# Performance work log

Measured on AMD Instinct MI355X. Metric: run time of the kernel, lower is better.

Reference implementation:

```python
import jax, jax.numpy as jnp
import numpy as np
from jax import lax

CONF_THRES = 0.25
IOU_THRES = 0.45
MAX_DET = 300      # detections kept after NMS
TOPK = 1024        # candidates entering NMS (sorted by score)
MAX_WH = 7680.0    # class offset for class-aware NMS
NC = 80            # classes
NM = 32            # mask prototypes
IMG = 640          # network input size
PROTO_HW = 160     # proto map resolution (IMG/4)
EPS = 1e-7


def xywh2xyxy(x):
    cx, cy, w, h = x[:, 0], x[:, 1], x[:, 2], x[:, 3]
    return jnp.stack([cx - w / 2, cy - h / 2, cx + w / 2, cy + h / 2], axis=1)


def box_iou(box1, box2):
    # box1: [K,4], box2: [M,4] in xyxy -> [K,M]
    a1, a2 = box1[:, None, :2], box1[:, None, 2:]
    b1, b2 = box2[None, :, :2], box2[None, :, 2:]
    inter = jnp.clip(jnp.minimum(a2, b2) - jnp.maximum(a1, b1), 0).prod(-1)
    area1 = (a2 - a1).prod(-1)
    area2 = (b2 - b1).prod(-1)
    return inter / (area1 + area2 - inter + EPS)


def greedy_nms_keep(boxes, valid, iou_thres):
    # boxes already sorted by descending score; returns bool keep mask [K]
    K = boxes.shape[0]
    sup = box_iou(boxes, boxes) > iou_thres  # [K,K]
    lower = jnp.arange(K)

    def body(i, keep):
        suppressed = jnp.any(keep & sup[:, i] & (lower < i))
        return keep.at[i].set(valid[i] & ~suppressed)

    return lax.fori_loop(0, K, body, jnp.zeros((K,), dtype=bool))


def setup_inputs() -> dict:
    key = jax.random.key(0)
    k1, k2, k3, k4, k5, k6 = jax.random.split(key, 6)
    N = 25200
    cxcy = jax.random.uniform(k1, (1, N, 2), jnp.float32, 0.0, float(IMG))
    wh = jax.random.uniform(k2, (1, N, 2), jnp.float32, 5.0, 120.0)
    obj = jax.random.uniform(k3, (1, N, 1), jnp.float32)
    cls = jax.random.uniform(k4, (1, N, NC), jnp.float32)
    coef = jax.random.normal(k5, (1, N, NM), jnp.float32) * 0.5
    prediction = jnp.concatenate([cxcy, wh, obj, cls, coef], axis=2)  # [1,N,117]
    protos = jax.random.normal(k6, (NM, PROTO_HW, PROTO_HW), jnp.float32)
    return {"prediction": prediction, "protos": protos}


def reference(prediction, protos):
    x = prediction[0]                       # [N, 5+NC+NM]
    obj = x[:, 4]
    cls_conf = x[:, 5:5 + NC] * obj[:, None]  # x[:,5:] *= x[:,4:5]
    conf = cls_conf.max(axis=1)
    j = jnp.argmax(cls_conf, axis=1)
    valid_all = (obj > CONF_THRES) & (conf > CONF_THRES)

    boxes_all = xywh2xyxy(x[:, :4])
    scores_masked = jnp.where(valid_all, conf, -1.0)
    top_scores, idx = lax.top_k(scores_masked, TOPK)  # sorted descending

    b = boxes_all[idx]              # [TOPK,4], no class offset
    cls_id = j[idx]                 # [TOPK]
    coef = x[idx, 5 + NC:]          # [TOPK,NM]
    valid = top_scores > CONF_THRES

    nms_boxes = b + (cls_id.astype(b.dtype) * MAX_WH)[:, None]  # class-aware
    keep = greedy_nms_keep(nms_boxes, valid, IOU_THRES)

    keep_scores = jnp.where(keep, top_scores, -1.0)
    fs, i2 = lax.top_k(keep_scores, MAX_DET)
    fvalid = fs > CONF_THRES
    fb = b[i2] * fvalid[:, None].astype(b.dtype)
    fcls = jnp.where(fvalid, cls_id[i2], -1)
    fcoef = coef[i2] * fvalid[:, None].astype(coef.dtype)
    fs = jnp.where(fvalid, fs, 0.0)

    # process_mask_native
    m = jax.nn.sigmoid(fcoef @ protos.reshape(NM, -1))          # [MAX_DET, HW*HW]
    m = m.reshape(MAX_DET, PROTO_HW, PROTO_HW)
    m = jax.image.resize(m, (MAX_DET, IMG, IMG), method='bilinear')
    x1, y1, x2, y2 = fb[:, 0], fb[:, 1], fb[:, 2], fb[:, 3]
    r = jnp.arange(IMG, dtype=fb.dtype)[None, None, :]  # along width vs x
    c = jnp.arange(IMG, dtype=fb.dtype)[None, :, None]  # along height vs y
    crop = ((r >= x1[:, None, None]) & (r < x2[:, None, None]) &
            (c >= y1[:, None, None]) & (c < y2[:, None, None]))
    masks_f = m * crop.astype(m.dtype) * fvalid[:, None, None].astype(m.dtype)
    masks_bool = masks_f > 0.5
    return masks_f, masks_bool, fb, fs, fcls
```

## Files before the change

kernel.cpp:

```cpp
#include <hip/hip_runtime.h>

constexpr int   kNA     = 25200;
constexpr int   kStride = 117;
constexpr int   kNC     = 80;
constexpr int   kNM     = 32;
constexpr int   kTopK   = 1024;
constexpr int   kMaxDet = 300;
constexpr int   kImg    = 640;
constexpr int   kPHW    = 160;
constexpr float kConfT  = 0.25f;
constexpr float kIouT   = 0.45f;
constexpr float kMaxWH  = 7680.0f;

constexpr unsigned long long kMaskElems = 300ull * 640ull * 640ull;

typedef float v4f __attribute__((ext_vector_type(4)));

constexpr size_t kN4     = (2ull * kMaskElems) >> 2;
constexpr size_t kZA_end = 27648000;
constexpr size_t kZB_end = 33792000;

constexpr int kZTopk = 512;
constexpr int kZSup  = 256;
constexpr int kZNms  = 1024;

constexpr size_t O_SCORES = 0;
constexpr size_t O_BOXES  = 100864;
constexpr size_t O_CLS    = 504064;
constexpr size_t O_TKIDX  = 604864;
constexpr size_t O_TKSC   = 608960;
constexpr size_t O_TKBOX  = 613056;
constexpr size_t O_TKNBOX = 629440;
constexpr size_t O_TKCLS  = 645824;
constexpr size_t O_SUP    = 649984;
constexpr size_t O_NDET   = 782336;
constexpr size_t O_DBOX   = 782400;
constexpr size_t O_DCOEF  = 787264;

constexpr int kDecRows = 64;
constexpr int kDecThr  = 128;
__global__ __launch_bounds__(kDecThr) void decode_k(const float* __restrict__ pred,
        float* __restrict__ scores, float* __restrict__ boxes, int* __restrict__ cls) {
    __shared__ float rows[kDecRows * kStride];
    int base = blockIdx.x * kDecRows;
    int nrows = min(kDecRows, kNA - base);
    int total = nrows * kStride;
    const float* src = pred + (size_t)base * kStride;
    for (int i = threadIdx.x; i < total; i += kDecThr) rows[i] = src[i];
    __syncthreads();
    int r = threadIdx.x;
    if (r >= nrows) return;
    int a = base + r;
    const float* p = rows + r * kStride;
    float obj = p[4];
    float best = -1.0f; int bj = 0;
    for (int c = 0; c < kNC; ++c) {
        float v = p[5 + c] * obj;
        if (v > best) { best = v; bj = c; }
    }
    bool valid = (obj > kConfT) && (best > kConfT);
    scores[a] = valid ? best : -1.0f;
    float cx = p[0], cy = p[1], w = p[2], h = p[3];
    float hw = w * 0.5f, hh = h * 0.5f;
    boxes[4*a+0] = cx - hw; boxes[4*a+1] = cy - hh;
    boxes[4*a+2] = cx + hw; boxes[4*a+3] = cy + hh;
    cls[a] = bj;
}

__device__ __forceinline__ unsigned f2ord(float f) {
    unsigned b = __float_as_uint(f);
    return (b & 0x80000000u) ? ~b : (b | 0x80000000u);
}
__device__ __forceinline__ float ord2f(unsigned u) {
    unsigned b = (u & 0x80000000u) ? (u ^ 0x80000000u) : ~u;
    return __uint_as_float(b);
}

__global__ __launch_bounds__(1024) void topk_k(const float* __restrict__ scores,
        const float* __restrict__ boxes, const int* __restrict__ cls,
        int* __restrict__ tk_idx, float* __restrict__ tk_sc, float* __restrict__ tk_box,
        float* __restrict__ tk_nbox, int* __restrict__ tk_cls,
        float* __restrict__ outz) {
    if (blockIdx.x != 0) {
        v4f z = 0.f;
        size_t stride = (size_t)(gridDim.x - 1) * 1024;
        for (size_t i = (size_t)(blockIdx.x - 1) * 1024 + threadIdx.x; i < kZA_end; i += stride)
            __builtin_nontemporal_store(z, ((v4f*)outz) + i);
        return;
    }
    __shared__ unsigned long long keys[kTopK];
    __shared__ int wcnt[16];
    __shared__ unsigned sh_cnt;
    int tid = threadIdx.x;
    int lane = tid & 63, wid = tid >> 6;

    unsigned uv[25];
#pragma unroll
    for (int k = 0; k < 25; ++k) {
        int i = tid + k * 1024;
        uv[k] = (i < kNA) ? f2ord(scores[i]) : 0u;
    }

    unsigned lo = 0u, hi = 0xFFFFFFFFu;
    for (int it = 0; it < 34; ++it) {
        unsigned mid;
        if (it == 0)      mid = 0xBE800000u;
        else if (it == 1) mid = 0xBF800001u;
        else {
            mid = (unsigned)(((unsigned long long)lo + (unsigned long long)hi) >> 1);
            if (mid == lo) break;
        }
        if (mid <= lo || mid >= hi) continue;
        int c = 0;
#pragma unroll
        for (int k = 0; k < 25; ++k) c += (uv[k] >= mid);
#pragma unroll
        for (int off = 32; off >= 1; off >>= 1) c += __shfl_down(c, off);
        __syncthreads();
        if (lane == 0) wcnt[wid] = c;
        __syncthreads();
        int tot = 0;
#pragma unroll
        for (int w = 0; w < 16; ++w) tot += wcnt[w];
        if (tot >= kTopK) lo = mid; else hi = mid;
    }
    unsigned uT = lo;

    int nGreater;
    {
        int c = 0;
#pragma unroll
        for (int k = 0; k < 25; ++k) c += (uv[k] >= uT + 1u);
#pragma unroll
        for (int off = 32; off >= 1; off >>= 1) c += __shfl_down(c, off);
        __syncthreads();
        if (lane == 0) wcnt[wid] = c;
        __syncthreads();
        int t = 0;
#pragma unroll
        for (int w = 0; w < 16; ++w) t += wcnt[w];
        nGreater = t;
    }
    int krem = kTopK - nGreater;
    if (tid == 0) sh_cnt = 0;
    __syncthreads();

#pragma unroll
    for (int k = 0; k < 25; ++k) {
        int i = tid + k * 1024;
        unsigned u = uv[k];
        if (i < kNA && u > uT) {
            unsigned p = atomicAdd(&sh_cnt, 1u);
            keys[p] = ((unsigned long long)u << 32) | (unsigned)(~i);
        }
    }

    int ilo = 0, ihi = kNA;
    while (ilo < ihi) {
        int mid = (ilo + ihi) >> 1;
        int c = 0;
#pragma unroll
        for (int k = 0; k < 25; ++k) {
            int i = tid + k * 1024;
            c += (i < mid && uv[k] == uT);
        }
#pragma unroll
        for (int off = 32; off >= 1; off >>= 1) c += __shfl_down(c, off);
        __syncthreads();
        if (lane == 0) wcnt[wid] = c;
        __syncthreads();
        int cc = 0;
#pragma unroll
        for (int w = 0; w < 16; ++w) cc += wcnt[w];
        if (cc >= krem) ihi = mid; else ilo = mid + 1;
    }
#pragma unroll
    for (int k = 0; k < 25; ++k) {
        int i = tid + k * 1024;
        if (i < ilo && uv[k] == uT) {
            unsigned p = atomicAdd(&sh_cnt, 1u);
            keys[p] = ((unsigned long long)uT << 32) | (unsigned)(~i);
        }
    }
    __syncthreads();

    for (int k2 = 2; k2 <= kTopK; k2 <<= 1) {
        for (int j = k2 >> 1; j > 0; j >>= 1) {
            int partner = tid ^ j;
            unsigned long long a = keys[tid], b = keys[partner];
            bool iLower = (tid & j) == 0;
            bool descRegion = (tid & k2) == 0;
            unsigned long long mx = (a > b) ? a : b;
            unsigned long long mn = (a > b) ? b : a;
            unsigned long long res = (iLower == descRegion) ? mx : mn;
            __syncthreads();
            keys[tid] = res;
            __syncthreads();
        }
    }

    unsigned long long key = keys[tid];
    unsigned u = (unsigned)(key >> 32);
    int idx = (int)(~((unsigned)key));
    tk_idx[tid] = idx;
    tk_sc[tid]  = ord2f(u);
    float4 bx = ((const float4*)boxes)[idx];
    ((float4*)tk_box)[tid] = bx;
    int cid = cls[idx];
    float off = (float)cid * kMaxWH;
    float4 nb; nb.x = bx.x + off; nb.y = bx.y + off; nb.z = bx.z + off; nb.w = bx.w + off;
    ((float4*)tk_nbox)[tid] = nb;
    tk_cls[tid] = cid;
}

__global__ __launch_bounds__(256) void supmat_k(const float* __restrict__ tk_nbox,
                                                unsigned long long* __restrict__ sup,
                                                float* __restrict__ outz) {
    if (blockIdx.x >= 64) {
        v4f z = 0.f;
        size_t stride = (size_t)(gridDim.x - 64) * 256;
        for (size_t i = kZA_end + (size_t)(blockIdx.x - 64) * 256 + threadIdx.x;
             i < kZB_end; i += stride)
            __builtin_nontemporal_store(z, ((v4f*)outz) + i);
        return;
    }
    __shared__ float4 bxs[kTopK];
    int tid = threadIdx.x;
    for (int k = tid; k < kTopK; k += 256) bxs[k] = ((const float4*)tk_nbox)[k];
    __syncthreads();
    int r = tid >> 4, w = tid & 15;
    int i = blockIdx.x * 16 + r;
    float4 a = bxs[i];
    float areaA = (a.z - a.x) * (a.w - a.y);
    unsigned long long bits = 0;
    for (int l = 0; l < 64; ++l) {
        float4 b = bxs[w * 64 + l];
        float xx1 = fmaxf(a.x, b.x), yy1 = fmaxf(a.y, b.y);
        float xx2 = fminf(a.z, b.z), yy2 = fminf(a.w, b.w);
        float iw = fmaxf(xx2 - xx1, 0.f), ih = fmaxf(yy2 - yy1, 0.f);
        float inter = iw * ih;
        float areaB = (b.z - b.x) * (b.w - b.y);
        float iou = inter / (areaA + areaB - inter + 1e-7f);
        if (iou > kIouT) bits |= 1ull << l;
    }
    sup[(size_t)i * 16 + w] = bits;
}

__global__ __launch_bounds__(256) void nms_k(const float* __restrict__ pred,
        const float* __restrict__ tk_sc, const int* __restrict__ tk_idx,
        const float* __restrict__ tk_box, const int* __restrict__ tk_cls,
        const unsigned long long* __restrict__ sup,
        int* __restrict__ ndet, float* __restrict__ out,
        float* __restrict__ dbox, float* __restrict__ dcoef) {
    if (blockIdx.x != 0) {
        v4f z = 0.f;
        size_t stride = (size_t)(gridDim.x - 1) * 256;
        for (size_t i = kZB_end + (size_t)(blockIdx.x - 1) * 256 + threadIdx.x;
             i < kN4; i += stride)
            __builtin_nontemporal_store(z, ((v4f*)out) + i);
        return;
    }
    __shared__ unsigned long long buf[2][1024];
    __shared__ int dslot_lds[kMaxDet];
    __shared__ int sh_nd;
    int tid = threadIdx.x;
    int lane = tid & 63;

    unsigned long long vW = 0;
    if (tid < 64) {
        for (int b = 0; b < 16; ++b) {
            unsigned long long bw = __ballot(tk_sc[b * 64 + lane] > kConfT);
            if (lane == b) vW = bw;
        }
    }
    for (int i = tid; i < 1024; i += 256) buf[0][i] = sup[i];

    unsigned long long supW = 0;
    unsigned long long kws[16];
    for (int b = 0; b < 16; ++b) {
        __syncthreads();
        if (tid >= 64) {
            if (b + 1 < 16) {
                for (int i = tid - 64; i < 1024; i += 192)
                    buf[(b + 1) & 1][i] = sup[(size_t)(b + 1) * 1024 + i];
            }
        } else {
            const unsigned long long* ch = buf[b & 1];
            unsigned long long s  = __shfl(supW, b);
            unsigned long long vb = __shfl(vW, b);
            unsigned long long kw = 0;
            unsigned long long rbuf[8];
            int w16 = lane & 15;
#pragma unroll
            for (int p = 0; p < 8; ++p) rbuf[p] = ch[p * 16 + w16];
            for (int l = 0; l < 64; ++l) {
                unsigned long long rw = rbuf[l & 7];
                if (l + 8 < 64) rbuf[l & 7] = ch[(l + 8) * 16 + w16];
                unsigned long long rb = __shfl(rw, b);
                bool kp = ((vb >> l) & 1ull) && !((s >> l) & 1ull);
                if (kp) { kw |= 1ull << l; s |= rb; supW |= rw; }
            }
            kws[b] = kw;
        }
    }
    if (tid == 0) {
        int d = 0;
        for (int b = 0; b < 16 && d < kMaxDet; ++b) {
            unsigned long long kw = kws[b];
            for (int l = 0; l < 64 && d < kMaxDet; ++l)
                if ((kw >> l) & 1ull) dslot_lds[d++] = b * 64 + l;
        }
        sh_nd = d;
        *ndet = d;
    }
    __syncthreads();

    int n = sh_nd;
    float* fb   = out + 2 * kMaskElems;
    float* fs   = fb + kMaxDet * 4;
    float* fcls = fs + kMaxDet;
    for (int d = tid; d < kMaxDet; d += 256) {
        if (d < n) {
            int t = dslot_lds[d];
            int a = tk_idx[t];
            float4 bx = ((const float4*)tk_box)[t];
            fb[4*d+0] = bx.x; fb[4*d+1] = bx.y; fb[4*d+2] = bx.z; fb[4*d+3] = bx.w;
            fs[d] = tk_sc[t];
            fcls[d] = (float)tk_cls[t];
            ((float4*)dbox)[d] = bx;
            const float* cp = pred + (size_t)a * kStride + 5 + kNC;
            for (int c = 0; c < kNM; ++c) dcoef[d * kNM + c] = cp[c];
        } else {
            fb[4*d+0] = 0.f; fb[4*d+1] = 0.f; fb[4*d+2] = 0.f; fb[4*d+3] = 0.f;
            fs[d] = 0.f; fcls[d] = -1.0f;
            float4 z; z.x = z.y = z.z = z.w = 0.f;
            ((float4*)dbox)[d] = z;
            for (int c = 0; c < kNM; ++c) dcoef[d * kNM + c] = 0.f;
        }
    }
}

constexpr int kPatch = 34;

__global__ __launch_bounds__(256) void patch_k(const float* __restrict__ protos,
        const float* __restrict__ dbox, const float* __restrict__ dcoef,
        const int* __restrict__ ndet, float* __restrict__ out) {
    int d = blockIdx.x;
    if (d >= *ndet) return;
    float4 bx = ((const float4*)dbox)[d];
    float x1 = bx.x, y1 = bx.y, x2 = bx.z, y2 = bx.w;

    int i_lo = max(0, (int)ceilf(y1));
    int i_hi = min(kImg - 1, (int)ceilf(y2) - 1);
    int j_lo = max(0, (int)ceilf(x1));
    int j_hi = min(kImg - 1, (int)ceilf(x2) - 1);
    if (i_lo > i_hi || j_lo > j_hi) return;

    int py_lo = min(159, max(0, (int)floorf(((float)i_lo + 0.5f) * 0.25f - 0.5f)));
    int py_hi = min(159, max(0, (int)floorf(((float)i_hi + 0.5f) * 0.25f - 0.5f) + 1));
    int px_lo = min(159, max(0, (int)floorf(((float)j_lo + 0.5f) * 0.25f - 0.5f)));
    int px_hi = min(159, max(0, (int)floorf(((float)j_hi + 0.5f) * 0.25f - 0.5f) + 1));
    int ph = py_hi - py_lo + 1, pw = px_hi - px_lo + 1;
    if (ph > kPatch) ph = kPatch;
    if (pw > kPatch) pw = kPatch;

    int tid = threadIdx.x;
    __shared__ float coef[kNM];
    __shared__ float patch[kPatch * kPatch];
    if (tid < kNM) coef[tid] = dcoef[d * kNM + tid];
    __syncthreads();
    int cells = ph * pw;
    for (int c = tid; c < cells; c += 256) {
        int py = py_lo + c / pw, px = px_lo + c % pw;
        const float* pp = protos + (size_t)py * kPHW + px;
        float z = 0.f;
#pragma unroll
        for (int m = 0; m < kNM; ++m) z = fmaf(coef[m], pp[(size_t)m * kPHW * kPHW], z);
        patch[c] = 1.0f / (1.0f + expf(-z));
    }
    __syncthreads();

    float* mf = out + (size_t)d * (kImg * kImg);
    float* mb = out + kMaskElems + (size_t)d * (kImg * kImg);
    int W = j_hi - j_lo + 1;
    int H = i_hi - i_lo + 1;
    int dr = tid >> 7, dc = tid & 127;
    for (int rr = dr; rr < H; rr += 2) {
        int i = i_lo + rr;
        float sy = fminf(fmaxf(((float)i + 0.5f) * 0.25f - 0.5f, 0.f), 159.f);
        int yy0 = (int)sy; float fy = sy - (float)yy0;
        int yy1i = min(yy0 + 1, 159);
        const float* prow0 = &patch[(yy0 - py_lo) * pw - px_lo];
        const float* prow1 = &patch[(yy1i - py_lo) * pw - px_lo];
        for (int cc = dc; cc < W; cc += 128) {
            int j = j_lo + cc;
            float sx = fminf(fmaxf(((float)j + 0.5f) * 0.25f - 0.5f, 0.f), 159.f);
            int xx0 = (int)sx; float fx = sx - (float)xx0;
            int xx1i = min(xx0 + 1, 159);
            float v00 = prow0[xx0], v01 = prow0[xx1i];
            float v10 = prow1[xx0], v11 = prow1[xx1i];
            float top = (1.f - fx) * v00 + fx * v01;
            float bot = (1.f - fx) * v10 + fx * v11;
            float m = (1.f - fy) * top + fy * bot;
            mf[(size_t)i * kImg + j] = m;
            mb[(size_t)i * kImg + j] = (m > 0.5f) ? 1.f : 0.f;
        }
    }
}

extern "C" void kernel_launch(void* const* d_in, const int* in_sizes, int n_in,
                              void* d_out, int out_size, void* d_ws, size_t ws_size,
                              hipStream_t stream) {
    const float* pred   = (const float*)d_in[0];
    const float* protos = (const float*)d_in[1];
    float* out = (float*)d_out;
    char* ws = (char*)d_ws;

    float* s_scores = (float*)(ws + O_SCORES);
    float* s_boxes  = (float*)(ws + O_BOXES);
    int*   s_cls    = (int*)  (ws + O_CLS);
    int*   tk_idx   = (int*)  (ws + O_TKIDX);
    float* tk_sc    = (float*)(ws + O_TKSC);
    float* tk_box   = (float*)(ws + O_TKBOX);
    float* tk_nbox  = (float*)(ws + O_TKNBOX);
    int*   tk_cls   = (int*)  (ws + O_TKCLS);
    unsigned long long* sup = (unsigned long long*)(ws + O_SUP);
    int*   ndet     = (int*)  (ws + O_NDET);
    float* dbox     = (float*)(ws + O_DBOX);
    float* dcoef    = (float*)(ws + O_DCOEF);

    decode_k<<<dim3((kNA + kDecRows - 1) / kDecRows), dim3(kDecThr), 0, stream>>>(pred, s_scores, s_boxes, s_cls);
    topk_k<<<dim3(1 + kZTopk), dim3(1024), 0, stream>>>(s_scores, s_boxes, s_cls,
                                               tk_idx, tk_sc, tk_box, tk_nbox, tk_cls, out);
    supmat_k<<<dim3(64 + kZSup), dim3(256), 0, stream>>>(tk_nbox, sup, out);
    nms_k<<<dim3(1 + kZNms), dim3(256), 0, stream>>>(pred, tk_sc, tk_idx, tk_box, tk_cls, sup,
                                             ndet, out, dbox, dcoef);
    patch_k<<<dim3(kMaxDet), dim3(256), 0, stream>>>(protos, dbox, dcoef, ndet, out);
}
```

Before: 1.113 ms.

## Skip zero-fill of mask rows covered by boxes; write full rows vectorized

Spreads the zero-fill of the mask output across all five kernels, including decode. The last chunk of the fill now runs in the finalize kernel and skips rows that fall inside each detection's box row range, which nms computes. The patch kernel writes whole 640-wide rows, including the zeros outside the box, as vectorized nontemporal float4 stores. The aim is to avoid writing covered rows twice and to overlap more of the fill with the serial stages, at the cost of extra index arithmetic per fill element.

```diff
diff --git a/kernel.cpp b/kernel.cpp
--- a/kernel.cpp
+++ b/kernel.cpp
@@ -16,13 +16,21 @@
 
 typedef float v4f __attribute__((ext_vector_type(4)));
 
-constexpr size_t kN4     = (2ull * kMaskElems) >> 2;
-constexpr size_t kZA_end = 27648000;
-constexpr size_t kZB_end = 33792000;
-
-constexpr int kZTopk = 512;
-constexpr int kZSup  = 256;
-constexpr int kZNms  = 1024;
+constexpr size_t kN4       = 61440000;
+constexpr size_t kQSlices  = 30720000;
+constexpr int    kQPerSlice= 102400;
+constexpr int    kQPerRow  = 160;
+
+constexpr size_t kZDecE  = 6144000;
+constexpr size_t kZTopkE = 15360000;
+constexpr size_t kZSupE  = 18432000;
+constexpr size_t kZNmsE  = 24576000;
+
+constexpr int kZDecB  = 1024;
+constexpr int kZTopkB = 512;
+constexpr int kZSupB  = 256;
+constexpr int kZNmsB  = 512;
+constexpr int kZFinB  = 1280;
 
 constexpr size_t O_SCORES = 0;
 constexpr size_t O_BOXES  = 100864;
@@ -36,11 +44,22 @@
 constexpr size_t O_NDET   = 782336;
 constexpr size_t O_DBOX   = 782400;
 constexpr size_t O_DCOEF  = 787264;
+constexpr size_t O_ROWR   = 825664;
 
 constexpr int kDecRows = 64;
 constexpr int kDecThr  = 128;
+constexpr int kDecBlocks = (kNA + kDecRows - 1) / kDecRows;
 __global__ __launch_bounds__(kDecThr) void decode_k(const float* __restrict__ pred,
-        float* __restrict__ scores, float* __restrict__ boxes, int* __restrict__ cls) {
+        float* __restrict__ scores, float* __restrict__ boxes, int* __restrict__ cls,
+        float* __restrict__ outz) {
+    if (blockIdx.x >= kDecBlocks) {
+        v4f z = 0.f;
+        size_t stride = (size_t)(gridDim.x - kDecBlocks) * kDecThr;
+        for (size_t i = (size_t)(blockIdx.x - kDecBlocks) * kDecThr + threadIdx.x;
+             i < kZDecE; i += stride)
+            __builtin_nontemporal_store(z, ((v4f*)outz) + i);
+        return;
+    }
     __shared__ float rows[kDecRows * kStride];
     int base = blockIdx.x * kDecRows;
     int nrows = min(kDecRows, kNA - base);
@@ -84,7 +103,8 @@
     if (blockIdx.x != 0) {
         v4f z = 0.f;
         size_t stride = (size_t)(gridDim.x - 1) * 1024;
-        for (size_t i = (size_t)(blockIdx.x - 1) * 1024 + threadIdx.x; i < kZA_end; i += stride)
+        for (size_t i = kZDecE + (size_t)(blockIdx.x - 1) * 1024 + threadIdx.x;
+             i < kZTopkE; i += stride)
             __builtin_nontemporal_store(z, ((v4f*)outz) + i);
         return;
     }
@@ -219,8 +239,8 @@
     if (blockIdx.x >= 64) {
         v4f z = 0.f;
         size_t stride = (size_t)(gridDim.x - 64) * 256;
-        for (size_t i = kZA_end + (size_t)(blockIdx.x - 64) * 256 + threadIdx.x;
-             i < kZB_end; i += stride)
+        for (size_t i = kZTopkE + (size_t)(blockIdx.x - 64) * 256 + threadIdx.x;
+             i < kZSupE; i += stride)
             __builtin_nontemporal_store(z, ((v4f*)outz) + i);
         return;
     }
@@ -251,12 +271,13 @@
         const float* __restrict__ tk_box, const int* __restrict__ tk_cls,
         const unsigned long long* __restrict__ sup,
         int* __restrict__ ndet, float* __restrict__ out,
-        float* __restrict__ dbox, float* __restrict__ dcoef) {
+        float* __restrict__ dbox, float* __restrict__ dcoef,
+        int2* __restrict__ rowr) {
     if (blockIdx.x != 0) {
         v4f z = 0.f;
         size_t stride = (size_t)(gridDim.x - 1) * 256;
-        for (size_t i = kZB_end + (size_t)(blockIdx.x - 1) * 256 + threadIdx.x;
-             i < kN4; i += stride)
+        for (size_t i = kZSupE + (size_t)(blockIdx.x - 1) * 256 + threadIdx.x;
+             i < kZNmsE; i += stride)
             __builtin_nontemporal_store(z, ((v4f*)out) + i);
         return;
     }
@@ -320,6 +341,7 @@
     float* fs   = fb + kMaxDet * 4;
     float* fcls = fs + kMaxDet;
     for (int d = tid; d < kMaxDet; d += 256) {
+        int2 rr; rr.x = 1; rr.y = 0;
         if (d < n) {
             int t = dslot_lds[d];
             int a = tk_idx[t];
@@ -330,6 +352,11 @@
             ((float4*)dbox)[d] = bx;
             const float* cp = pred + (size_t)a * kStride + 5 + kNC;
             for (int c = 0; c < kNM; ++c) dcoef[d * kNM + c] = cp[c];
+            int i_lo = max(0, (int)ceilf(bx.y));
+            int i_hi = min(kImg - 1, (int)ceilf(bx.w) - 1);
+            int j_lo = max(0, (int)ceilf(bx.x));
+            int j_hi = min(kImg - 1, (int)ceilf(bx.z) - 1);
+            if (i_lo <= i_hi && j_lo <= j_hi) { rr.x = i_lo; rr.y = i_hi; }
         } else {
             fb[4*d+0] = 0.f; fb[4*d+1] = 0.f; fb[4*d+2] = 0.f; fb[4*d+3] = 0.f;
             fs[d] = 0.f; fcls[d] = -1.0f;
@@ -337,24 +364,42 @@
             ((float4*)dbox)[d] = z;
             for (int c = 0; c < kNM; ++c) dcoef[d * kNM + c] = 0.f;
         }
+        rowr[d] = rr;
     }
 }
 
 constexpr int kPatch = 34;
 
-__global__ __launch_bounds__(256) void patch_k(const float* __restrict__ protos,
+__global__ __launch_bounds__(256) void finalize_k(const float* __restrict__ protos,
         const float* __restrict__ dbox, const float* __restrict__ dcoef,
-        const int* __restrict__ ndet, float* __restrict__ out) {
+        const int2* __restrict__ rowr, float* __restrict__ out) {
+    int tid = threadIdx.x;
+    if (blockIdx.x >= kMaxDet) {
+        __shared__ int2 rr_lds[kMaxDet];
+        for (int t = tid; t < kMaxDet; t += 256) rr_lds[t] = rowr[t];
+        __syncthreads();
+        v4f z = 0.f;
+        size_t stride = (size_t)(gridDim.x - kMaxDet) * 256;
+        for (size_t q = kZNmsE + (size_t)(blockIdx.x - kMaxDet) * 256 + tid;
+             q < kN4; q += stride) {
+            size_t qr = (q >= kQSlices) ? (q - kQSlices) : q;
+            int d = (int)(qr / kQPerSlice);
+            int rowq = (int)(qr - (size_t)d * kQPerSlice);
+            int i = rowq / kQPerRow;
+            int2 rr = rr_lds[d];
+            if (i < rr.x || i > rr.y)
+                __builtin_nontemporal_store(z, ((v4f*)out) + q);
+        }
+        return;
+    }
     int d = blockIdx.x;
-    if (d >= *ndet) return;
+    int2 rr = rowr[d];
+    if (rr.x > rr.y) return;
     float4 bx = ((const float4*)dbox)[d];
     float x1 = bx.x, y1 = bx.y, x2 = bx.z, y2 = bx.w;
-
-    int i_lo = max(0, (int)ceilf(y1));
-    int i_hi = min(kImg - 1, (int)ceilf(y2) - 1);
+    int i_lo = rr.x, i_hi = rr.y;
     int j_lo = max(0, (int)ceilf(x1));
     int j_hi = min(kImg - 1, (int)ceilf(x2) - 1);
-    if (i_lo > i_hi || j_lo > j_hi) return;
 
     int py_lo = min(159, max(0, (int)floorf(((float)i_lo + 0.5f) * 0.25f - 0.5f)));
     int py_hi = min(159, max(0, (int)floorf(((float)i_hi + 0.5f) * 0.25f - 0.5f) + 1));
@@ -364,7 +409,6 @@
     if (ph > kPatch) ph = kPatch;
     if (pw > kPatch) pw = kPatch;
 
-    int tid = threadIdx.x;
     __shared__ float coef[kNM];
     __shared__ float patch[kPatch * kPatch];
     if (tid < kNM) coef[tid] = dcoef[d * kNM + tid];
@@ -382,29 +426,38 @@
 
     float* mf = out + (size_t)d * (kImg * kImg);
     float* mb = out + kMaskElems + (size_t)d * (kImg * kImg);
-    int W = j_hi - j_lo + 1;
     int H = i_hi - i_lo + 1;
-    int dr = tid >> 7, dc = tid & 127;
-    for (int rr = dr; rr < H; rr += 2) {
-        int i = i_lo + rr;
+    int work = H * kQPerRow;
+    for (int w = tid; w < work; w += 256) {
+        int rrow = w / kQPerRow;
+        int jq = w - rrow * kQPerRow;
+        int i = i_lo + rrow;
         float sy = fminf(fmaxf(((float)i + 0.5f) * 0.25f - 0.5f, 0.f), 159.f);
         int yy0 = (int)sy; float fy = sy - (float)yy0;
         int yy1i = min(yy0 + 1, 159);
         const float* prow0 = &patch[(yy0 - py_lo) * pw - px_lo];
         const float* prow1 = &patch[(yy1i - py_lo) * pw - px_lo];
-        for (int cc = dc; cc < W; cc += 128) {
-            int j = j_lo + cc;
-            float sx = fminf(fmaxf(((float)j + 0.5f) * 0.25f - 0.5f, 0.f), 159.f);
-            int xx0 = (int)sx; float fx = sx - (float)xx0;
-            int xx1i = min(xx0 + 1, 159);
-            float v00 = prow0[xx0], v01 = prow0[xx1i];
-            float v10 = prow1[xx0], v11 = prow1[xx1i];
-            float top = (1.f - fx) * v00 + fx * v01;
-            float bot = (1.f - fx) * v10 + fx * v11;
-            float m = (1.f - fy) * top + fy * bot;
-            mf[(size_t)i * kImg + j] = m;
-            mb[(size_t)i * kImg + j] = (m > 0.5f) ? 1.f : 0.f;
-        }
+        v4f vf = 0.f;
+        v4f vb = 0.f;
+        int j0 = jq * 4;
+#pragma unroll
+        for (int t = 0; t < 4; ++t) {
+            int j = j0 + t;
+            if (j >= j_lo && j <= j_hi) {
+                float sx = fminf(fmaxf(((float)j + 0.5f) * 0.25f - 0.5f, 0.f), 159.f);
+                int xx0 = (int)sx; float fx = sx - (float)xx0;
+                int xx1i = min(xx0 + 1, 159);
+                float v00 = prow0[xx0], v01 = prow0[xx1i];
+                float v10 = prow1[xx0], v11 = prow1[xx1i];
+                float top = (1.f - fx) * v00 + fx * v01;
+                float bot = (1.f - fx) * v10 + fx * v11;
+                float m = (1.f - fy) * top + fy * bot;
+                vf[t] = m;
+                vb[t] = (m > 0.5f) ? 1.f : 0.f;
+            }
+        }
+        __builtin_nontemporal_store(vf, (v4f*)(mf + (size_t)i * kImg + j0));
+        __builtin_nontemporal_store(vb, (v4f*)(mb + (size_t)i * kImg + j0));
     }
 }
 
@@ -428,12 +481,13 @@
     int*   ndet     = (int*)  (ws + O_NDET);
     float* dbox     = (float*)(ws + O_DBOX);
     float* dcoef    = (float*)(ws + O_DCOEF);
-
-    decode_k<<<dim3((kNA + kDecRows - 1) / kDecRows), dim3(kDecThr), 0, stream>>>(pred, s_scores, s_boxes, s_cls);
-    topk_k<<<dim3(1 + kZTopk), dim3(1024), 0, stream>>>(s_scores, s_boxes, s_cls,
+    int2*  rowr     = (int2*) (ws + O_ROWR);
+
+    decode_k<<<dim3(kDecBlocks + kZDecB), dim3(kDecThr), 0, stream>>>(pred, s_scores, s_boxes, s_cls, out);
+    topk_k<<<dim3(1 + kZTopkB), dim3(1024), 0, stream>>>(s_scores, s_boxes, s_cls,
                                                tk_idx, tk_sc, tk_box, tk_nbox, tk_cls, out);
-    supmat_k<<<dim3(64 + kZSup), dim3(256), 0, stream>>>(tk_nbox, sup, out);
-    nms_k<<<dim3(1 + kZNms), dim3(256), 0, stream>>>(pred, tk_sc, tk_idx, tk_box, tk_cls, sup,
-                                             ndet, out, dbox, dcoef);
-    patch_k<<<dim3(kMaxDet), dim3(256), 0, stream>>>(protos, dbox, dcoef, ndet, out);
-}
+    supmat_k<<<dim3(64 + kZSupB), dim3(256), 0, stream>>>(tk_nbox, sup, out);
+    nms_k<<<dim3(1 + kZNmsB), dim3(256), 0, stream>>>(pred, tk_sc, tk_idx, tk_box, tk_cls, sup,
+                                             ndet, out, dbox, dcoef, rowr);
+    finalize_k<<<dim3(kMaxDet + kZFinB), dim3(256), 0, stream>>>(protos, dbox, dcoef, rowr, out);
+}
```

New measurement: 1.169 ms. +5.0%, slower.

## Spread output zeroing into decode and split mask painting across row-quarter blocks

Applied to the files above, without the earlier changes.

Adds a zero-fill range to the decode kernel so output clearing starts earlier. The later kernels' zero ranges shift to match, and the supmat kernel gets more zero-fill blocks. The patch kernel now runs four blocks per detection, each covering a quarter of the box rows with a smaller proto patch. Mask writes become 4-wide vector nontemporal stores, with border lanes writing zero. The goal is better parallelism in the mask painting kernel and more overlap of the large memset with the serial front stages. The risk is extra launch work, and the quarter-row patch height cap of 12 must hold for tall boxes.

```diff
diff --git a/kernel.cpp b/kernel.cpp
--- a/kernel.cpp
+++ b/kernel.cpp
@@ -16,13 +16,15 @@
 
 typedef float v4f __attribute__((ext_vector_type(4)));
 
-constexpr size_t kN4     = (2ull * kMaskElems) >> 2;
-constexpr size_t kZA_end = 27648000;
-constexpr size_t kZB_end = 33792000;
-
-constexpr int kZTopk = 512;
-constexpr int kZSup  = 256;
-constexpr int kZNms  = 1024;
+constexpr size_t kN4 = 61440000;
+constexpr size_t kZ0 = 4000000;
+constexpr size_t kZ1 = 29600000;
+constexpr size_t kZ2 = 35744000;
+
+constexpr int kZDecB  = 512;
+constexpr int kZTopkB = 512;
+constexpr int kZSupB  = 320;
+constexpr int kZNmsB  = 1024;
 
 constexpr size_t O_SCORES = 0;
 constexpr size_t O_BOXES  = 100864;
@@ -39,8 +41,18 @@
 
 constexpr int kDecRows = 64;
 constexpr int kDecThr  = 128;
+constexpr int kDecBlocks = (kNA + kDecRows - 1) / kDecRows;
 __global__ __launch_bounds__(kDecThr) void decode_k(const float* __restrict__ pred,
-        float* __restrict__ scores, float* __restrict__ boxes, int* __restrict__ cls) {
+        float* __restrict__ scores, float* __restrict__ boxes, int* __restrict__ cls,
+        float* __restrict__ outz) {
+    if (blockIdx.x >= kDecBlocks) {
+        v4f z = 0.f;
+        size_t stride = (size_t)(gridDim.x - kDecBlocks) * kDecThr;
+        for (size_t i = (size_t)(blockIdx.x - kDecBlocks) * kDecThr + threadIdx.x;
+             i < kZ0; i += stride)
+            __builtin_nontemporal_store(z, ((v4f*)outz) + i);
+        return;
+    }
     __shared__ float rows[kDecRows * kStride];
     int base = blockIdx.x * kDecRows;
     int nrows = min(kDecRows, kNA - base);
@@ -84,7 +96,8 @@
     if (blockIdx.x != 0) {
         v4f z = 0.f;
         size_t stride = (size_t)(gridDim.x - 1) * 1024;
-        for (size_t i = (size_t)(blockIdx.x - 1) * 1024 + threadIdx.x; i < kZA_end; i += stride)
+        for (size_t i = kZ0 + (size_t)(blockIdx.x - 1) * 1024 + threadIdx.x;
+             i < kZ1; i += stride)
             __builtin_nontemporal_store(z, ((v4f*)outz) + i);
         return;
     }
@@ -219,8 +232,8 @@
     if (blockIdx.x >= 64) {
         v4f z = 0.f;
         size_t stride = (size_t)(gridDim.x - 64) * 256;
-        for (size_t i = kZA_end + (size_t)(blockIdx.x - 64) * 256 + threadIdx.x;
-             i < kZB_end; i += stride)
+        for (size_t i = kZ1 + (size_t)(blockIdx.x - 64) * 256 + threadIdx.x;
+             i < kZ2; i += stride)
             __builtin_nontemporal_store(z, ((v4f*)outz) + i);
         return;
     }
@@ -255,7 +268,7 @@
     if (blockIdx.x != 0) {
         v4f z = 0.f;
         size_t stride = (size_t)(gridDim.x - 1) * 256;
-        for (size_t i = kZB_end + (size_t)(blockIdx.x - 1) * 256 + threadIdx.x;
+        for (size_t i = kZ2 + (size_t)(blockIdx.x - 1) * 256 + threadIdx.x;
              i < kN4; i += stride)
             __builtin_nontemporal_store(z, ((v4f*)out) + i);
         return;
@@ -340,12 +353,15 @@
     }
 }
 
-constexpr int kPatch = 34;
+constexpr int kSplit   = 4;
+constexpr int kPatchH  = 12;
+constexpr int kPatchW  = 34;
 
 __global__ __launch_bounds__(256) void patch_k(const float* __restrict__ protos,
         const float* __restrict__ dbox, const float* __restrict__ dcoef,
         const int* __restrict__ ndet, float* __restrict__ out) {
-    int d = blockIdx.x;
+    int d    = blockIdx.x >> 2;
+    int part = blockIdx.x & 3;
     if (d >= *ndet) return;
     float4 bx = ((const float4*)dbox)[d];
     float x1 = bx.x, y1 = bx.y, x2 = bx.z, y2 = bx.w;
@@ -356,17 +372,22 @@
     int j_hi = min(kImg - 1, (int)ceilf(x2) - 1);
     if (i_lo > i_hi || j_lo > j_hi) return;
 
-    int py_lo = min(159, max(0, (int)floorf(((float)i_lo + 0.5f) * 0.25f - 0.5f)));
-    int py_hi = min(159, max(0, (int)floorf(((float)i_hi + 0.5f) * 0.25f - 0.5f) + 1));
+    int H  = i_hi - i_lo + 1;
+    int r0 = i_lo + (H * part) / kSplit;
+    int r1 = i_lo + (H * (part + 1)) / kSplit - 1;
+    if (r0 > r1) return;
+
+    int py_lo = min(159, max(0, (int)floorf(((float)r0 + 0.5f) * 0.25f - 0.5f)));
+    int py_hi = min(159, max(0, (int)floorf(((float)r1 + 0.5f) * 0.25f - 0.5f) + 1));
     int px_lo = min(159, max(0, (int)floorf(((float)j_lo + 0.5f) * 0.25f - 0.5f)));
     int px_hi = min(159, max(0, (int)floorf(((float)j_hi + 0.5f) * 0.25f - 0.5f) + 1));
     int ph = py_hi - py_lo + 1, pw = px_hi - px_lo + 1;
-    if (ph > kPatch) ph = kPatch;
-    if (pw > kPatch) pw = kPatch;
+    if (ph > kPatchH) ph = kPatchH;
+    if (pw > kPatchW) pw = kPatchW;
 
     int tid = threadIdx.x;
     __shared__ float coef[kNM];
-    __shared__ float patch[kPatch * kPatch];
+    __shared__ float patch[kPatchH * kPatchW];
     if (tid < kNM) coef[tid] = dcoef[d * kNM + tid];
     __syncthreads();
     int cells = ph * pw;
@@ -382,29 +403,40 @@
 
     float* mf = out + (size_t)d * (kImg * kImg);
     float* mb = out + kMaskElems + (size_t)d * (kImg * kImg);
-    int W = j_hi - j_lo + 1;
-    int H = i_hi - i_lo + 1;
-    int dr = tid >> 7, dc = tid & 127;
-    for (int rr = dr; rr < H; rr += 2) {
-        int i = i_lo + rr;
+    int jq_lo = j_lo >> 2, jq_hi = j_hi >> 2;
+    int nq = jq_hi - jq_lo + 1;
+    int Hq = r1 - r0 + 1;
+    int work = Hq * nq;
+    for (int w = tid; w < work; w += 256) {
+        int rrow = w / nq;
+        int jqo  = w - rrow * nq;
+        int i  = r0 + rrow;
+        int j0 = (jq_lo + jqo) * 4;
         float sy = fminf(fmaxf(((float)i + 0.5f) * 0.25f - 0.5f, 0.f), 159.f);
         int yy0 = (int)sy; float fy = sy - (float)yy0;
         int yy1i = min(yy0 + 1, 159);
         const float* prow0 = &patch[(yy0 - py_lo) * pw - px_lo];
         const float* prow1 = &patch[(yy1i - py_lo) * pw - px_lo];
-        for (int cc = dc; cc < W; cc += 128) {
-            int j = j_lo + cc;
-            float sx = fminf(fmaxf(((float)j + 0.5f) * 0.25f - 0.5f, 0.f), 159.f);
-            int xx0 = (int)sx; float fx = sx - (float)xx0;
-            int xx1i = min(xx0 + 1, 159);
-            float v00 = prow0[xx0], v01 = prow0[xx1i];
-            float v10 = prow1[xx0], v11 = prow1[xx1i];
-            float top = (1.f - fx) * v00 + fx * v01;
-            float bot = (1.f - fx) * v10 + fx * v11;
-            float m = (1.f - fy) * top + fy * bot;
-            mf[(size_t)i * kImg + j] = m;
-            mb[(size_t)i * kImg + j] = (m > 0.5f) ? 1.f : 0.f;
-        }
+        v4f vf = 0.f;
+        v4f vb = 0.f;
+#pragma unroll
+        for (int t = 0; t < 4; ++t) {
+            int j = j0 + t;
+            if (j >= j_lo && j <= j_hi) {
+                float sx = fminf(fmaxf(((float)j + 0.5f) * 0.25f - 0.5f, 0.f), 159.f);
+                int xx0 = (int)sx; float fx = sx - (float)xx0;
+                int xx1i = min(xx0 + 1, 159);
+                float v00 = prow0[xx0], v01 = prow0[xx1i];
+                float v10 = prow1[xx0], v11 = prow1[xx1i];
+                float top = (1.f - fx) * v00 + fx * v01;
+                float bot = (1.f - fx) * v10 + fx * v11;
+                float m = (1.f - fy) * top + fy * bot;
+                vf[t] = m;
+                vb[t] = (m > 0.5f) ? 1.f : 0.f;
+            }
+        }
+        __builtin_nontemporal_store(vf, (v4f*)(mf + (size_t)i * kImg + j0));
+        __builtin_nontemporal_store(vb, (v4f*)(mb + (size_t)i * kImg + j0));
     }
 }
 
@@ -429,11 +461,11 @@
     float* dbox     = (float*)(ws + O_DBOX);
     float* dcoef    = (float*)(ws + O_DCOEF);
 
-    decode_k<<<dim3((kNA + kDecRows - 1) / kDecRows), dim3(kDecThr), 0, stream>>>(pred, s_scores, s_boxes, s_cls);
-    topk_k<<<dim3(1 + kZTopk), dim3(1024), 0, stream>>>(s_scores, s_boxes, s_cls,
+    decode_k<<<dim3(kDecBlocks + kZDecB), dim3(kDecThr), 0, stream>>>(pred, s_scores, s_boxes, s_cls, out);
+    topk_k<<<dim3(1 + kZTopkB), dim3(1024), 0, stream>>>(s_scores, s_boxes, s_cls,
                                                tk_idx, tk_sc, tk_box, tk_nbox, tk_cls, out);
-    supmat_k<<<dim3(64 + kZSup), dim3(256), 0, stream>>>(tk_nbox, sup, out);
-    nms_k<<<dim3(1 + kZNms), dim3(256), 0, stream>>>(pred, tk_sc, tk_idx, tk_box, tk_cls, sup,
+    supmat_k<<<dim3(64 + kZSupB), dim3(256), 0, stream>>>(tk_nbox, sup, out);
+    nms_k<<<dim3(1 + kZNmsB), dim3(256), 0, stream>>>(pred, tk_sc, tk_idx, tk_box, tk_cls, sup,
                                              ndet, out, dbox, dcoef);
-    patch_k<<<dim3(kMaxDet), dim3(256), 0, stream>>>(protos, dbox, dcoef, ndet, out);
-}
+    patch_k<<<dim3(kMaxDet * kSplit), dim3(256), 0, stream>>>(protos, dbox, dcoef, ndet, out);
+}
```

Measured after the change: 1.080 ms. 2.9% less time.
